# Kernel optimization log

Hardware: AMD Instinct MI355X
Metric: run time of the kernel (lower is better)

Reference implementation:

```python
import jax, jax.numpy as jnp
import numpy as np

B, IN, H = 8192, 1024, 1024


def setup_inputs() -> dict:
    key = jax.random.key(0)
    kx, kh, kc, kwx, kwh = jax.random.split(key, 5)
    return {
        "x": jax.random.normal(kx, (B, IN), dtype=jnp.float32),
        "h": jax.random.normal(kh, (B, H), dtype=jnp.float32),
        "c": jax.random.normal(kc, (B, H), dtype=jnp.float32),
        # 8 Dense layers fused: gate order [i, f, g, o] along last axis
        "Wx": jax.random.normal(kwx, (IN, 4 * H), dtype=jnp.float32) * 0.02,
        "Wh": jax.random.normal(kwh, (H, 4 * H), dtype=jnp.float32) * 0.02,
        "bx": jnp.zeros((4 * H,), dtype=jnp.float32),
        "bh": jnp.zeros((4 * H,), dtype=jnp.float32),
    }


def reference(x, h, c, Wx, Wh, bx, bh):
    # Fused equivalent of the 8 separate Dense layers:
    #   gate_k = x @ Wx[:, k] + bx[k] + h @ Wh[:, k] + bh[k]
    gates = x @ Wx + h @ Wh + (bx + bh)  # [B, 4H]
    i, f, g, o = jnp.split(gates, 4, axis=-1)
    i = jax.nn.sigmoid(i)
    f = jax.nn.sigmoid(f)
    g = jnp.tanh(g)
    o = jax.nn.sigmoid(o)
    c_new = f * c + i * g
    h_new = o * jnp.tanh(c_new)
    # Original returns (out_gate, hidden_state, cell_state)
    return (o, h_new, c_new)
```

## Files before the change

kernel.cpp:

```cpp
#include <hip/hip_runtime.h>
#include <hip/hip_bf16.h>

typedef __attribute__((ext_vector_type(8))) short bf16x8;
typedef __attribute__((ext_vector_type(4))) float f32x4;
typedef __attribute__((ext_vector_type(8))) unsigned short u16x8;

#define B_DIM 8192
#define H_DIM 1024
#define K_DIM 2048
#define N_DIM 4096
#define BH (B_DIM * H_DIM)

__device__ __forceinline__ unsigned short f2bf(float f) {
    union { float f; unsigned u; } v; v.f = f;
    unsigned r = v.u + 0x7FFFu + ((v.u >> 16) & 1u);
    return (unsigned short)(r >> 16);
}

__device__ __forceinline__ void gload16(const void* g, void* l) {
    __builtin_amdgcn_global_load_lds(
        (const __attribute__((address_space(1))) void*)g,
        (__attribute__((address_space(3))) void*)l, 16, 0, 0);
}

__global__ void prep(const float* __restrict__ x, const float* __restrict__ h,
                     const float* __restrict__ Wx, const float* __restrict__ Wh,
                     unsigned short* __restrict__ Abf, unsigned short* __restrict__ Bperm) {
    __shared__ float tile[64][65];
    const int t = threadIdx.x;
    if (blockIdx.x < 8192) {
        int gid = blockIdx.x * 256 + t;
        size_t e = (size_t)gid * 8;
        int m   = gid >> 8;
        int col = (gid & 255) * 8;
        int p   = col >> 10;
        int k   = col & 1023;
        const float* src = (p ? h : x) + (size_t)m * 1024 + k;
        float4 v0 = *(const float4*)src;
        float4 v1 = *(const float4*)(src + 4);
        u16x8 o = { f2bf(v0.x), f2bf(v0.y), f2bf(v0.z), f2bf(v0.w),
                    f2bf(v1.x), f2bf(v1.y), f2bf(v1.z), f2bf(v1.w) };
        *(u16x8*)(Abf + e) = o;
        return;
    }
    const int bz = blockIdx.x - 8192;
    const int k0 = (bz & 31) * 64;
    const int n0 = (bz >> 5) * 64;
#pragma unroll
    for (int it = 0; it < 4; ++it) {
        int lin = it * 256 + t;
        int kl  = lin >> 4;
        int n4  = lin & 15;
        int k   = k0 + kl;
        const float* src = (k < 1024) ? (Wx + (size_t)k * 4096 + n0 + n4 * 4)
                                      : (Wh + (size_t)(k - 1024) * 4096 + n0 + n4 * 4);
        float4 v = *(const float4*)src;
        tile[kl][n4 * 4 + 0] = v.x;
        tile[kl][n4 * 4 + 1] = v.y;
        tile[kl][n4 * 4 + 2] = v.z;
        tile[kl][n4 * 4 + 3] = v.w;
    }
    __syncthreads();
#pragma unroll
    for (int it = 0; it < 2; ++it) {
        int lin = it * 256 + t;
        int nl  = lin >> 3;
        int ch  = lin & 7;
        int n    = n0 + nl;
        int gate = n >> 10;
        int j    = n & 1023;
        int jb   = j >> 5;
        int jj   = j & 31;
        int R    = jb * 128 + (jj >> 4) * 64 + gate * 16 + (jj & 15);
        u16x8 o;
#pragma unroll
        for (int q = 0; q < 8; ++q) o[q] = f2bf(tile[ch * 8 + q][nl]);
        *(u16x8*)(Bperm + (size_t)R * 2048 + k0 + ch * 8) = o;
    }
}

__global__ __launch_bounds__(256, 4) void lstm_fused(
    const unsigned short* __restrict__ Abf,
    const unsigned short* __restrict__ Bperm,
    const float* __restrict__ bx, const float* __restrict__ bh,
    const float* __restrict__ cin, float* __restrict__ out) {
    __shared__ unsigned short lsA[128 * 64];
    __shared__ unsigned short lsB[128 * 64];

    const int tid  = threadIdx.x;
    const int wave = tid >> 6;
    const int lane = tid & 63;
    const int m0 = blockIdx.x * 128;
    const int jb = blockIdx.y;
    const int wm = wave >> 1;
    const int wn = wave & 1;

    f32x4 acc[4][4];
#pragma unroll
    for (int i = 0; i < 4; ++i)
#pragma unroll
        for (int j = 0; j < 4; ++j) acc[i][j] = (f32x4){0.f, 0.f, 0.f, 0.f};

    const int sRow   = tid >> 3;
    const int sChunk = (((tid & 7) ^ ((tid >> 3) & 7))) * 8;
    const int aBase = (m0 + sRow) * K_DIM + sChunk;
    const int bBase = (jb * 128 + sRow) * K_DIM + sChunk;

    const int fRow  = lane & 15;
    const int qBase = lane >> 4;
    const int rx    = fRow & 7;

    for (int kt = 0; kt < 32; ++kt) {
        const int kOff = kt * 64;
#pragma unroll
        for (int it = 0; it < 4; ++it) {
            gload16(Abf + aBase + it * (32 * K_DIM) + kOff, lsA + it * 2048 + wave * 512);
            gload16(Bperm + bBase + it * (32 * K_DIM) + kOff, lsB + it * 2048 + wave * 512);
        }
        __syncthreads();
#pragma unroll
        for (int ks = 0; ks < 2; ++ks) {
            bf16x8 af[4], bfr[4];
            const int qPhys = (ks * 4 + qBase) ^ rx;
#pragma unroll
            for (int tm = 0; tm < 4; ++tm)
                af[tm] = *(const bf16x8*)(lsA + (wm * 64 + tm * 16 + fRow) * 64 + qPhys * 8);
#pragma unroll
            for (int tn = 0; tn < 4; ++tn)
                bfr[tn] = *(const bf16x8*)(lsB + (wn * 64 + tn * 16 + fRow) * 64 + qPhys * 8);
#pragma unroll
            for (int tm = 0; tm < 4; ++tm)
#pragma unroll
                for (int tn = 0; tn < 4; ++tn)
                    acc[tm][tn] = __builtin_amdgcn_mfma_f32_16x16x32_bf16(
                        af[tm], bfr[tn], acc[tm][tn], 0, 0, 0);
        }
        __syncthreads();
    }

    const int j = jb * 32 + wn * 16 + fRow;
    const float b_i = bx[j] + bh[j];
    const float b_f = bx[1024 + j] + bh[1024 + j];
    const float b_g = bx[2048 + j] + bh[2048 + j];
    const float b_o = bx[3072 + j] + bh[3072 + j];
#pragma unroll
    for (int tm = 0; tm < 4; ++tm) {
#pragma unroll
        for (int r = 0; r < 4; ++r) {
            const int row = m0 + wm * 64 + tm * 16 + (lane >> 4) * 4 + r;
            float vi = acc[tm][0][r] + b_i;
            float vf = acc[tm][1][r] + b_f;
            float vg = acc[tm][2][r] + b_g;
            float vo = acc[tm][3][r] + b_o;
            float ig = 1.f / (1.f + __expf(-vi));
            float fg = 1.f / (1.f + __expf(-vf));
            float e2g = __expf(2.f * fminf(fmaxf(vg, -15.f), 15.f));
            float gg = (e2g - 1.f) / (e2g + 1.f);
            float og = 1.f / (1.f + __expf(-vo));
            float cn = fg * cin[(size_t)row * 1024 + j] + ig * gg;
            float e2c = __expf(2.f * fminf(fmaxf(cn, -15.f), 15.f));
            float hn = og * ((e2c - 1.f) / (e2c + 1.f));
            out[(size_t)row * 1024 + j] = og;
            out[(size_t)BH + (size_t)row * 1024 + j] = hn;
            out[(size_t)2 * BH + (size_t)row * 1024 + j] = cn;
        }
    }
}

extern "C" void kernel_launch(void* const* d_in, const int* in_sizes, int n_in,
                              void* d_out, int out_size, void* d_ws, size_t ws_size,
                              hipStream_t stream) {
    const float* x  = (const float*)d_in[0];
    const float* h  = (const float*)d_in[1];
    const float* c  = (const float*)d_in[2];
    const float* Wx = (const float*)d_in[3];
    const float* Wh = (const float*)d_in[4];
    const float* bx = (const float*)d_in[5];
    const float* bh = (const float*)d_in[6];
    float* out = (float*)d_out;

    unsigned short* Abf   = (unsigned short*)d_ws;
    unsigned short* Bperm = (unsigned short*)((char*)d_ws + (size_t)B_DIM * K_DIM * 2);

    hipLaunchKernelGGL(prep, dim3(8192 + 2048), dim3(256), 0, stream, x, h, Wx, Wh, Abf, Bperm);
    hipLaunchKernelGGL(lstm_fused, dim3(B_DIM / 128, 32), dim3(256), 0, stream,
                       Abf, Bperm, bx, bh, c, out);
}
```

Baseline: 339.1 us.

## Use 256x256 tiles with double-buffered LDS ping-pong pipeline and block swizzle

Result: slower. 353.7 us (+4.3%).

```diff
diff --git a/kernel.cpp b/kernel.cpp
--- a/kernel.cpp
+++ b/kernel.cpp
@@ -10,6 +10,7 @@
 #define K_DIM 2048
 #define N_DIM 4096
 #define BH (B_DIM * H_DIM)
+#define NT 32
 
 __device__ __forceinline__ unsigned short f2bf(float f) {
     union { float f; unsigned u; } v; v.f = f;
@@ -79,75 +80,160 @@
     }
 }
 
-__global__ __launch_bounds__(256, 4) void lstm_fused(
+#define VMW(N) asm volatile("s_waitcnt vmcnt(" #N ")" ::: "memory")
+#define BAR() __builtin_amdgcn_s_barrier()
+
+#define LD_A(BUF, TMB) do { \
+  _Pragma("unroll") \
+  for (int _tm = 0; _tm < 4; ++_tm) \
+    _Pragma("unroll") \
+    for (int _ks = 0; _ks < 2; ++_ks) \
+      af[(TMB) + _tm][_ks] = *(const bf16x8*)(lsA + (BUF) * 16384 + \
+          (wm * 128 + ((TMB) + _tm) * 16 + fRow) * 64 + ((_ks * 4 + q4) ^ rx) * 8); \
+} while (0)
+
+#define LD_B(BUF, TNB) do { \
+  _Pragma("unroll") \
+  for (int _tn = 0; _tn < 2; ++_tn) \
+    _Pragma("unroll") \
+    for (int _ks = 0; _ks < 2; ++_ks) \
+      bfr[_tn][_ks] = *(const bf16x8*)(lsB + (BUF) * 16384 + \
+          (wn * 64 + ((TNB) + _tn) * 16 + fRow) * 64 + ((_ks * 4 + q4) ^ rx) * 8); \
+} while (0)
+
+#define STAGE_A(BUF, H, T) do { \
+  gload16(Abf + (size_t)(m0 + (H) * 128 + sRow) * K_DIM + (T) * 64 + sChunk, \
+          lsA + (BUF) * 16384 + (H) * 8192 + wave * 512); \
+  gload16(Abf + (size_t)(m0 + (H) * 128 + 64 + sRow) * K_DIM + (T) * 64 + sChunk, \
+          lsA + (BUF) * 16384 + (H) * 8192 + 4096 + wave * 512); \
+} while (0)
+
+#define STAGE_B(BUF, H, T) do { \
+  gload16(Bperm + (size_t)(r0 + (H) * 128 + sRow) * K_DIM + (T) * 64 + sChunk, \
+          lsB + (BUF) * 16384 + (H) * 8192 + wave * 512); \
+  gload16(Bperm + (size_t)(r0 + (H) * 128 + 64 + sRow) * K_DIM + (T) * 64 + sChunk, \
+          lsB + (BUF) * 16384 + (H) * 8192 + 4096 + wave * 512); \
+} while (0)
+
+#define MFMA_QUAD(TMB, TNB) do { \
+  __builtin_amdgcn_s_setprio(1); \
+  _Pragma("unroll") \
+  for (int _ks = 0; _ks < 2; ++_ks) \
+    _Pragma("unroll") \
+    for (int _tm = 0; _tm < 4; ++_tm) \
+      _Pragma("unroll") \
+      for (int _tn = 0; _tn < 2; ++_tn) \
+        acc[(TMB) + _tm][(TNB) + _tn] = __builtin_amdgcn_mfma_f32_16x16x32_bf16( \
+            af[(TMB) + _tm][_ks], bfr[_tn][_ks], acc[(TMB) + _tm][(TNB) + _tn], 0, 0, 0); \
+  __builtin_amdgcn_s_setprio(0); \
+} while (0)
+
+__global__ __launch_bounds__(512, 2) void lstm_fused(
     const unsigned short* __restrict__ Abf,
     const unsigned short* __restrict__ Bperm,
     const float* __restrict__ bx, const float* __restrict__ bh,
     const float* __restrict__ cin, float* __restrict__ out) {
-    __shared__ unsigned short lsA[128 * 64];
-    __shared__ unsigned short lsB[128 * 64];
+    __shared__ unsigned short lsA[2 * 256 * 64];
+    __shared__ unsigned short lsB[2 * 256 * 64];
 
     const int tid  = threadIdx.x;
     const int wave = tid >> 6;
     const int lane = tid & 63;
-    const int m0 = blockIdx.x * 128;
-    const int jb = blockIdx.y;
-    const int wm = wave >> 1;
-    const int wn = wave & 1;
-
-    f32x4 acc[4][4];
-#pragma unroll
-    for (int i = 0; i < 4; ++i)
+    const int wm   = wave >> 2;
+    const int wn   = wave & 3;
+
+    const int bid = blockIdx.x;
+    const int swz = (bid & 7) * 64 + (bid >> 3);
+    const int bm  = swz & 31;
+    const int bn  = swz >> 5;
+    const int m0  = bm * 256;
+    const int r0  = bn * 256;
+
+    const int sRow   = tid >> 3;
+    const int sChunk = ((tid & 7) ^ ((tid >> 3) & 7)) * 8;
+
+    const int fRow = lane & 15;
+    const int q4   = lane >> 4;
+    const int rx   = fRow & 7;
+
+    f32x4 acc[8][4];
+#pragma unroll
+    for (int i = 0; i < 8; ++i)
 #pragma unroll
         for (int j = 0; j < 4; ++j) acc[i][j] = (f32x4){0.f, 0.f, 0.f, 0.f};
 
-    const int sRow   = tid >> 3;
-    const int sChunk = (((tid & 7) ^ ((tid >> 3) & 7))) * 8;
-    const int aBase = (m0 + sRow) * K_DIM + sChunk;
-    const int bBase = (jb * 128 + sRow) * K_DIM + sChunk;
-
-    const int fRow  = lane & 15;
-    const int qBase = lane >> 4;
-    const int rx    = fRow & 7;
-
-    for (int kt = 0; kt < 32; ++kt) {
-        const int kOff = kt * 64;
-#pragma unroll
-        for (int it = 0; it < 4; ++it) {
-            gload16(Abf + aBase + it * (32 * K_DIM) + kOff, lsA + it * 2048 + wave * 512);
-            gload16(Bperm + bBase + it * (32 * K_DIM) + kOff, lsB + it * 2048 + wave * 512);
-        }
-        __syncthreads();
-#pragma unroll
-        for (int ks = 0; ks < 2; ++ks) {
-            bf16x8 af[4], bfr[4];
-            const int qPhys = (ks * 4 + qBase) ^ rx;
-#pragma unroll
-            for (int tm = 0; tm < 4; ++tm)
-                af[tm] = *(const bf16x8*)(lsA + (wm * 64 + tm * 16 + fRow) * 64 + qPhys * 8);
-#pragma unroll
-            for (int tn = 0; tn < 4; ++tn)
-                bfr[tn] = *(const bf16x8*)(lsB + (wn * 64 + tn * 16 + fRow) * 64 + qPhys * 8);
-#pragma unroll
-            for (int tm = 0; tm < 4; ++tm)
-#pragma unroll
-                for (int tn = 0; tn < 4; ++tn)
-                    acc[tm][tn] = __builtin_amdgcn_mfma_f32_16x16x32_bf16(
-                        af[tm], bfr[tn], acc[tm][tn], 0, 0, 0);
-        }
-        __syncthreads();
-    }
-
-    const int j = jb * 32 + wn * 16 + fRow;
+    bf16x8 af[8][2];
+    bf16x8 bfr[2][2];
+
+    STAGE_A(0, 0, 0); STAGE_A(0, 1, 0); STAGE_B(0, 0, 0); STAGE_B(0, 1, 0);
+    STAGE_A(1, 0, 1); STAGE_A(1, 1, 1);
+    VMW(4);
+    BAR();
+
+    for (int i = 0; i < 15; ++i) {
+        const int t = 2 * i;
+        LD_A(0, 0); LD_B(0, 0);
+        STAGE_B(1, 0, t + 1);
+        BAR();
+        MFMA_QUAD(0, 0);
+        BAR();
+        LD_A(0, 4);
+        STAGE_B(1, 1, t + 1);
+        BAR();
+        MFMA_QUAD(4, 0);
+        BAR();
+        LD_B(0, 2);
+        STAGE_A(0, 0, t + 2);
+        BAR();
+        MFMA_QUAD(4, 2);
+        BAR();
+        STAGE_A(0, 1, t + 2);
+        BAR();
+        MFMA_QUAD(0, 2);
+        VMW(4);
+        BAR();
+        LD_A(1, 0); LD_B(1, 0);
+        STAGE_B(0, 0, t + 2);
+        BAR();
+        MFMA_QUAD(0, 0);
+        BAR();
+        LD_A(1, 4);
+        STAGE_B(0, 1, t + 2);
+        BAR();
+        MFMA_QUAD(4, 0);
+        BAR();
+        LD_B(1, 2);
+        STAGE_A(1, 0, t + 3);
+        BAR();
+        MFMA_QUAD(4, 2);
+        BAR();
+        STAGE_A(1, 1, t + 3);
+        BAR();
+        MFMA_QUAD(0, 2);
+        VMW(4);
+        BAR();
+    }
+
+    STAGE_B(1, 0, 31); STAGE_B(1, 1, 31);
+    LD_A(0, 0); LD_B(0, 0); MFMA_QUAD(0, 0);
+    LD_A(0, 4);             MFMA_QUAD(4, 0);
+    LD_B(0, 2);             MFMA_QUAD(4, 2); MFMA_QUAD(0, 2);
+    VMW(0);
+    BAR();
+    LD_A(1, 0); LD_B(1, 0); MFMA_QUAD(0, 0);
+    LD_A(1, 4);             MFMA_QUAD(4, 0);
+    LD_B(1, 2);             MFMA_QUAD(4, 2); MFMA_QUAD(0, 2);
+
+    const int j = bn * 64 + (wn >> 1) * 32 + (wn & 1) * 16 + fRow;
     const float b_i = bx[j] + bh[j];
     const float b_f = bx[1024 + j] + bh[1024 + j];
     const float b_g = bx[2048 + j] + bh[2048 + j];
     const float b_o = bx[3072 + j] + bh[3072 + j];
 #pragma unroll
-    for (int tm = 0; tm < 4; ++tm) {
+    for (int tm = 0; tm < 8; ++tm) {
 #pragma unroll
         for (int r = 0; r < 4; ++r) {
-            const int row = m0 + wm * 64 + tm * 16 + (lane >> 4) * 4 + r;
+            const int row = m0 + wm * 128 + tm * 16 + q4 * 4 + r;
             float vi = acc[tm][0][r] + b_i;
             float vf = acc[tm][1][r] + b_f;
             float vg = acc[tm][2][r] + b_g;
@@ -183,6 +269,6 @@
     unsigned short* Bperm = (unsigned short*)((char*)d_ws + (size_t)B_DIM * K_DIM * 2);
 
     hipLaunchKernelGGL(prep, dim3(8192 + 2048), dim3(256), 0, stream, x, h, Wx, Wh, Abf, Bperm);
-    hipLaunchKernelGGL(lstm_fused, dim3(B_DIM / 128, 32), dim3(256), 0, stream,
+    hipLaunchKernelGGL(lstm_fused, dim3(512), dim3(512), 0, stream,
                        Abf, Bperm, bx, bh, c, out);
 }
```
